# Kernel tuning notes

Measured on AMD Instinct MI355X. Metric: run time of the kernel, lower is better.

## Reference

```python
import jax, jax.numpy as jnp
import numpy as np

N_NODES = 100000
N_EDGES = 1250000
D_IN = 64
D_OUT = 64


def setup_inputs() -> dict:
    key = jax.random.key(0)
    k1, k2, k3, k4, k5, k6 = jax.random.split(key, 6)
    x = jax.random.normal(k1, (N_NODES, D_IN), dtype=jnp.float32)
    W_self = jax.random.normal(k2, (D_IN, D_OUT), dtype=jnp.float32) / np.sqrt(D_IN)
    W_neigh = jax.random.normal(k3, (D_IN, D_OUT), dtype=jnp.float32) / np.sqrt(D_IN)
    b = jax.random.normal(k4, (D_OUT,), dtype=jnp.float32) * 0.01
    src = jax.random.randint(k5, (N_EDGES,), 0, N_NODES, dtype=jnp.int32)
    dst = jnp.sort(jax.random.randint(k6, (N_EDGES,), 0, N_NODES, dtype=jnp.int32))
    return {"x": x, "W_self": W_self, "W_neigh": W_neigh, "b": b, "src": src, "dst": dst}


def reference(x, W_self, W_neigh, b, src, dst):
    # DGL SAGEConv (aggregator_type='mean'):
    #   h_neigh[v] = mean_{u in N(v)} x[u]   (0 if in-degree 0)
    #   out = x @ W_self + h_neigh @ W_neigh + b
    n_nodes = x.shape[0]
    msgs = x[src]  # [E, D_IN] gather of source features
    agg = jax.ops.segment_sum(msgs, dst, num_segments=n_nodes)  # [N, D_IN]
    deg = jax.ops.segment_sum(jnp.ones_like(dst, dtype=x.dtype), dst, num_segments=n_nodes)
    h_neigh = agg / jnp.maximum(deg, 1.0)[:, None]
    return x @ W_self + h_neigh @ W_neigh + b
```

## Files before the change

kernel.cpp:

```cpp
#include <hip/hip_runtime.h>
#include <hip/hip_fp16.h>

#define NN 100000
#define NE 1250000
#define D 64
#define NTILE 1563
#define NWID (NTILE * 4)

__device__ inline float2 cvt2(unsigned u) {
    __half2 h = __builtin_bit_cast(__half2, u);
    return __half22float2(h);
}
__device__ inline unsigned pack2(float a, float b) {
    __half2 h = __floats2half2_rn(a, b);
    return __builtin_bit_cast(unsigned, h);
}

__global__ __launch_bounds__(256) void k_rowptr(const int* __restrict__ dst,
                                                int* __restrict__ row_ptr) {
    const int i = blockIdx.x * 256 + threadIdx.x;
    if (i >= NE) return;
    const int d = dst[i];
    const int prev = (i == 0) ? -1 : dst[i - 1];
    for (int v = prev + 1; v <= d; ++v) row_ptr[v] = i;
    if (i == NE - 1) {
        for (int v = d + 1; v <= NN; ++v) row_ptr[v] = NE;
    }
}

__global__ __launch_bounds__(256) void k_gemm(const float* __restrict__ x,
                                              const float* __restrict__ Wself,
                                              const float* __restrict__ Wneigh,
                                              const float* __restrict__ b,
                                              float* __restrict__ z,
                                              __half* __restrict__ y) {
    const int lane = threadIdx.x & 63;
    const int wid = __builtin_amdgcn_readfirstlane(blockIdx.x * 4 + (threadIdx.x >> 6));
    if (wid >= NWID) return;
    const int tile = wid >> 2;
    const int sel = wid & 3;
    const int jh = (sel & 1) * 32;
    const float* __restrict__ W = (sel & 2) ? Wneigh : Wself;

    const int n = tile * 64 + lane;
    const int nc = (n < NN) ? n : (NN - 1);
    const float* __restrict__ xr = x + (size_t)nc * D;

    float acc[32];
    #pragma unroll
    for (int j = 0; j < 32; ++j) acc[j] = 0.0f;

    #pragma unroll 2
    for (int k4 = 0; k4 < D / 4; ++k4) {
        const float4 xv = *(const float4*)(xr + k4 * 4);
        const float xk[4] = {xv.x, xv.y, xv.z, xv.w};
        #pragma unroll
        for (int i = 0; i < 4; ++i) {
            const float* __restrict__ wr = W + (k4 * 4 + i) * D + jh;
            #pragma unroll
            for (int j = 0; j < 32; ++j) {
                acc[j] = fmaf(xk[i], wr[j], acc[j]);
            }
        }
    }

    if (n < NN) {
        if (sel & 2) {
            unsigned p[16];
            #pragma unroll
            for (int g = 0; g < 16; ++g) p[g] = pack2(acc[2 * g], acc[2 * g + 1]);
            uint4* __restrict__ yo = (uint4*)(y + (size_t)n * D + jh);
            #pragma unroll
            for (int g = 0; g < 4; ++g) {
                uint4 v;
                v.x = p[4 * g + 0]; v.y = p[4 * g + 1];
                v.z = p[4 * g + 2]; v.w = p[4 * g + 3];
                yo[g] = v;
            }
        } else {
            float* __restrict__ zo = z + (size_t)n * D + jh;
            const float* __restrict__ br = b + jh;
            #pragma unroll
            for (int g = 0; g < 8; ++g) {
                float4 v;
                v.x = acc[g * 4 + 0] + br[g * 4 + 0];
                v.y = acc[g * 4 + 1] + br[g * 4 + 1];
                v.z = acc[g * 4 + 2] + br[g * 4 + 2];
                v.w = acc[g * 4 + 3] + br[g * 4 + 3];
                *(float4*)(zo + g * 4) = v;
            }
        }
    }
}

__global__ __launch_bounds__(256) void k_aggr(const __half* __restrict__ y,
                                              const int* __restrict__ src,
                                              const int* __restrict__ row_ptr,
                                              float* __restrict__ out) {
    const int tid  = threadIdx.x;
    const int lane = tid & 63;
    const int sub  = lane >> 3;
    const int q    = lane & 7;
    const int v    = __builtin_amdgcn_readfirstlane(blockIdx.x * 4 + (tid >> 6));
    if (v >= NN) return;
    const int lo = row_ptr[v];
    const int hi = row_ptr[v + 1];

    float acc[8];
    #pragma unroll
    for (int i = 0; i < 8; ++i) acc[i] = 0.0f;

    for (int e0 = lo; e0 < hi; e0 += 32) {
        uint4 r[4];
        #pragma unroll
        for (int j = 0; j < 4; ++j) {
            const int e = e0 + j * 8 + sub;
            const int ec = (e < hi) ? e : lo;
            r[j] = *(const uint4*)(y + (size_t)src[ec] * D + q * 8);
        }
        #pragma unroll
        for (int j = 0; j < 4; ++j) {
            const int e = e0 + j * 8 + sub;
            if (e < hi) {
                const float2 f0 = cvt2(r[j].x), f1 = cvt2(r[j].y);
                const float2 f2 = cvt2(r[j].z), f3 = cvt2(r[j].w);
                acc[0] += f0.x; acc[1] += f0.y;
                acc[2] += f1.x; acc[3] += f1.y;
                acc[4] += f2.x; acc[5] += f2.y;
                acc[6] += f3.x; acc[7] += f3.y;
            }
        }
    }
    #pragma unroll
    for (int off = 8; off < 64; off <<= 1) {
        #pragma unroll
        for (int i = 0; i < 8; ++i) acc[i] += __shfl_xor(acc[i], off);
    }
    if (lane < 8) {
        const float inv = (hi > lo) ? 1.0f / (float)(hi - lo) : 0.0f;
        float4* op = (float4*)(out + (size_t)v * D + lane * 8);
        float4 o0 = op[0], o1 = op[1];
        o0.x += acc[0] * inv; o0.y += acc[1] * inv;
        o0.z += acc[2] * inv; o0.w += acc[3] * inv;
        o1.x += acc[4] * inv; o1.y += acc[5] * inv;
        o1.z += acc[6] * inv; o1.w += acc[7] * inv;
        op[0] = o0; op[1] = o1;
    }
}

extern "C" void kernel_launch(void* const* d_in, const int* in_sizes, int n_in,
                              void* d_out, int out_size, void* d_ws, size_t ws_size,
                              hipStream_t stream) {
    const float* x      = (const float*)d_in[0];
    const float* Wself  = (const float*)d_in[1];
    const float* Wneigh = (const float*)d_in[2];
    const float* b      = (const float*)d_in[3];
    const int*   src    = (const int*)d_in[4];
    const int*   dst    = (const int*)d_in[5];
    float* out = (float*)d_out;

    __half* y      = (__half*)d_ws;
    int*   row_ptr = (int*)((char*)d_ws + (size_t)NN * D * 2);

    k_rowptr<<<(NE + 255) / 256, 256, 0, stream>>>(dst, row_ptr);
    k_gemm<<<(NWID + 3) / 4, 256, 0, stream>>>(x, Wself, Wneigh, b, out, y);
    k_aggr<<<(NN + 3) / 4, 256, 0, stream>>>(y, src, row_ptr, out);
}
```

Measured before the change: 157.7 us.

## Remap aggregation to half-wave per node with per-lane feature pairs

The aggregation kernel now gives each node 32 lanes, with every lane owning two fp16 features. Each lane walks all of the node's edges sequentially, four at a time, and software-prefetches the next source indices. This removes the cross-lane shuffle reduction and the idle-lane waste on low-degree nodes, and it halves the block count. In exchange each gather is a 4-byte load rather than 16 bytes, so one edge row takes 32 small loads, and latency now depends on the per-node edge loop.

```diff
diff --git a/kernel.cpp b/kernel.cpp
--- a/kernel.cpp
+++ b/kernel.cpp
@@ -97,55 +97,46 @@
                                               const int* __restrict__ src,
                                               const int* __restrict__ row_ptr,
                                               float* __restrict__ out) {
-    const int tid  = threadIdx.x;
-    const int lane = tid & 63;
-    const int sub  = lane >> 3;
-    const int q    = lane & 7;
-    const int v    = __builtin_amdgcn_readfirstlane(blockIdx.x * 4 + (tid >> 6));
+    const int lane = threadIdx.x & 63;
+    const int half = lane >> 5;
+    const int w    = lane & 31;
+    const int wid  = blockIdx.x * 4 + (threadIdx.x >> 6);
+    const int v    = wid * 2 + half;
     if (v >= NN) return;
+
     const int lo = row_ptr[v];
     const int hi = row_ptr[v + 1];
+    const int deg = hi - lo;
 
-    float acc[8];
-    #pragma unroll
-    for (int i = 0; i < 8; ++i) acc[i] = 0.0f;
-
-    for (int e0 = lo; e0 < hi; e0 += 32) {
-        uint4 r[4];
+    float a0 = 0.0f, a1 = 0.0f;
+    if (deg > 0) {
+        const int last = hi - 1;
+        int sv[4];
         #pragma unroll
-        for (int j = 0; j < 4; ++j) {
-            const int e = e0 + j * 8 + sub;
-            const int ec = (e < hi) ? e : lo;
-            r[j] = *(const uint4*)(y + (size_t)src[ec] * D + q * 8);
-        }
-        #pragma unroll
-        for (int j = 0; j < 4; ++j) {
-            const int e = e0 + j * 8 + sub;
-            if (e < hi) {
-                const float2 f0 = cvt2(r[j].x), f1 = cvt2(r[j].y);
-                const float2 f2 = cvt2(r[j].z), f3 = cvt2(r[j].w);
-                acc[0] += f0.x; acc[1] += f0.y;
-                acc[2] += f1.x; acc[3] += f1.y;
-                acc[4] += f2.x; acc[5] += f2.y;
-                acc[6] += f3.x; acc[7] += f3.y;
+        for (int u = 0; u < 4; ++u) sv[u] = src[min(lo + u, last)];
+        for (int e = lo; e < hi; e += 4) {
+            unsigned r[4];
+            #pragma unroll
+            for (int u = 0; u < 4; ++u)
+                r[u] = *(const unsigned*)(y + (size_t)sv[u] * D + w * 2);
+            const int en = e + 4;
+            #pragma unroll
+            for (int u = 0; u < 4; ++u) sv[u] = src[min(en + u, last)];
+            #pragma unroll
+            for (int u = 0; u < 4; ++u) {
+                if (e + u < hi) {
+                    const float2 f = cvt2(r[u]);
+                    a0 += f.x; a1 += f.y;
+                }
             }
         }
     }
-    #pragma unroll
-    for (int off = 8; off < 64; off <<= 1) {
-        #pragma unroll
-        for (int i = 0; i < 8; ++i) acc[i] += __shfl_xor(acc[i], off);
-    }
-    if (lane < 8) {
-        const float inv = (hi > lo) ? 1.0f / (float)(hi - lo) : 0.0f;
-        float4* op = (float4*)(out + (size_t)v * D + lane * 8);
-        float4 o0 = op[0], o1 = op[1];
-        o0.x += acc[0] * inv; o0.y += acc[1] * inv;
-        o0.z += acc[2] * inv; o0.w += acc[3] * inv;
-        o1.x += acc[4] * inv; o1.y += acc[5] * inv;
-        o1.z += acc[6] * inv; o1.w += acc[7] * inv;
-        op[0] = o0; op[1] = o1;
-    }
+    const float inv = (deg > 0) ? 1.0f / (float)deg : 0.0f;
+    float2* op = (float2*)(out + (size_t)v * D + w * 2);
+    float2 o = *op;
+    o.x += a0 * inv;
+    o.y += a1 * inv;
+    *op = o;
 }
 
 extern "C" void kernel_launch(void* const* d_in, const int* in_sizes, int n_in,
@@ -164,5 +155,5 @@
 
     k_rowptr<<<(NE + 255) / 256, 256, 0, stream>>>(dst, row_ptr);
     k_gemm<<<(NWID + 3) / 4, 256, 0, stream>>>(x, Wself, Wneigh, b, out, y);
-    k_aggr<<<(NN + 3) / 4, 256, 0, stream>>>(y, src, row_ptr, out);
+    k_aggr<<<(NN + 7) / 8, 256, 0, stream>>>(y, src, row_ptr, out);
 }
```

Result: no change. 154.8 us (-1.8%).
